# Kernel tuning notes

Measured on AMD Instinct MI355X. Metric: run time of the kernel, lower is better.

Reference implementation:

```python
import jax, jax.numpy as jnp
import numpy as np

N = 100000   # nodes
E = 1600000  # edges (avg degree 16)
D = 128      # input_dim == output_dim (residual requires equality)
BN_EPS = 1e-5


def setup_inputs() -> dict:
    key = jax.random.key(0)
    ks = jax.random.split(key, 8)
    X = jax.random.normal(ks[0], (N, D), dtype=jnp.float32)
    E_X = jax.random.normal(ks[1], (E, D), dtype=jnp.float32)
    snorm_n = jax.random.uniform(ks[2], (N, 1), dtype=jnp.float32)
    snorm_e = jax.random.uniform(ks[3], (E, 1), dtype=jnp.float32)
    src = jax.random.randint(ks[4], (E,), 0, N, dtype=jnp.int32)
    dst = jax.random.randint(ks[5], (E,), 0, N, dtype=jnp.int32)
    # Linear A and B parameters (torch nn.Linear: y = x @ W.T + b)
    scale = 1.0 / np.sqrt(D)
    A_w = jax.random.uniform(ks[6], (D, D), dtype=jnp.float32, minval=-scale, maxval=scale)
    B_w = jax.random.uniform(ks[7], (D, D), dtype=jnp.float32, minval=-scale, maxval=scale)
    A_b = jnp.zeros((D,), jnp.float32)
    B_b = jnp.zeros((D,), jnp.float32)
    # BatchNorm1d affine params (training mode -> batch stats)
    gamma = jnp.ones((D,), jnp.float32)
    beta = jnp.zeros((D,), jnp.float32)
    return {"X": X, "E_X": E_X, "snorm_n": snorm_n, "snorm_e": snorm_e,
            "src": src, "dst": dst, "A_w": A_w, "A_b": A_b,
            "B_w": B_w, "B_b": B_b, "gamma": gamma, "beta": beta}


def reference(X, E_X, snorm_n, snorm_e, src, dst, A_w, A_b, B_w, B_b, gamma, beta):
    AX = X @ A_w.T + A_b                       # [N, D]
    BX = X @ B_w.T + B_b                       # [N, D]
    # message: gather BX at edge sources; reduce: sum into destinations
    msgs = BX[src]                             # [E, D] irregular gather
    agg = jax.ops.segment_sum(msgs, dst, num_segments=N)  # [N, D]
    # DGL custom reduce only fires for nodes with in-degree > 0;
    # zero-in-degree nodes keep H = X
    indeg = jax.ops.segment_sum(jnp.ones((E,), X.dtype), dst, num_segments=N)
    H = jnp.where(indeg[:, None] > 0, AX + agg, X)
    H = H * snorm_n
    # BatchNorm1d (training mode: biased batch statistics)
    mean = jnp.mean(H, axis=0)
    var = jnp.mean((H - mean) ** 2, axis=0)
    H = (H - mean) * jax.lax.rsqrt(var + BN_EPS) * gamma + beta
    H = jax.nn.relu(H)
    H = X + H                                  # residual
    return (H, E_X)
```

## Files before the change

### kernel.cpp

```cpp
#include <hip/hip_runtime.h>

#define D 128
#define NNODES 100000
#define NEDGES 1600000
#define BN_EPS 1e-5f
#define NB_STATS 2048
#define NBLK_P 391
#define NTILES 1563

#define OFF_AX     0
#define OFF_BX16   12800000
#define OFF_ESRC   19200000
#define OFF_ORDER  20800000
#define OFF_INDEG  22400000
#define OFF_LEXC   22620000
#define OFF_BPART  22730000
#define OFF_BSCAN  22731000
#define OFF_PSUM   22740000
#define OFF_PSQ    23010000
#define OFF_SCALE  23280000
#define OFF_SHIFT  23280128
#define WS_NEED_BYTES 93200000ull

#define MAIN_GEMM 512
#define MAIN_EDGE 2048
#define MAIN_AGG  2048
#define MAIN_FIN  2048

typedef __attribute__((ext_vector_type(8))) short bf16x8;
typedef __attribute__((ext_vector_type(4))) float f32x4;

static __device__ __forceinline__ unsigned short f2bf(float f) {
    unsigned int u = __float_as_uint(f);
    u = (u + 0x7FFF + ((u >> 16) & 1)) >> 16;
    return (unsigned short)u;
}
static __device__ __forceinline__ float bf_lo(unsigned v) {
    return __uint_as_float(v << 16);
}
static __device__ __forceinline__ float bf_hi(unsigned v) {
    return __uint_as_float(v & 0xFFFF0000u);
}
static __device__ __forceinline__ bf16x8 pack8(float4 a, float4 b) {
    union { uint4 u; bf16x8 v; } r;
    r.u.x = (unsigned)f2bf(a.x) | ((unsigned)f2bf(a.y) << 16);
    r.u.y = (unsigned)f2bf(a.z) | ((unsigned)f2bf(a.w) << 16);
    r.u.z = (unsigned)f2bf(b.x) | ((unsigned)f2bf(b.y) << 16);
    r.u.w = (unsigned)f2bf(b.z) | ((unsigned)f2bf(b.w) << 16);
    return r.v;
}

__global__ __launch_bounds__(256, 2) void gemm2_kernel(
    const float* __restrict__ X,
    const float* __restrict__ Aw, const float* __restrict__ Ab,
    const float* __restrict__ Bw, const float* __restrict__ Bb,
    float* __restrict__ AX, unsigned short* __restrict__ BX16)
{
    __shared__ unsigned short Xs[64][136];

    const int w    = threadIdx.x >> 6;
    const int lane = threadIdx.x & 63;
    const bool isB = (w >> 1);
    const int colbase = (w & 1) * 64;
    const int bn   = lane & 15;
    const int kg   = lane >> 4;

    const float* __restrict__ Wm   = isB ? Bw : Aw;
    const float* __restrict__ bias = isB ? Bb : Ab;

    bf16x8 wf[4][4];
#pragma unroll
    for (int ks = 0; ks < 4; ++ks)
#pragma unroll
        for (int ct = 0; ct < 4; ++ct) {
            const int d = colbase + ct * 16 + bn;
            const int k = ks * 32 + kg * 8;
            const float4* wp = (const float4*)&Wm[d * D + k];
            wf[ks][ct] = pack8(wp[0], wp[1]);
        }

    float bias4[4];
#pragma unroll
    for (int ct = 0; ct < 4; ++ct) bias4[ct] = bias[colbase + ct * 16 + bn];

    for (int t = blockIdx.x; t < NTILES; t += MAIN_GEMM) {
        const int row0 = t * 64;
        for (int c = threadIdx.x; c < 1024; c += 256) {
            const int r   = c >> 4;
            const int col = (c & 15) * 8;
            const int row = min(row0 + r, NNODES - 1);
            const float4* xp = (const float4*)&X[(size_t)row * D + col];
            const float4 x0 = xp[0], x1 = xp[1];
            union { uint4 u; } pk;
            pk.u.x = (unsigned)f2bf(x0.x) | ((unsigned)f2bf(x0.y) << 16);
            pk.u.y = (unsigned)f2bf(x0.z) | ((unsigned)f2bf(x0.w) << 16);
            pk.u.z = (unsigned)f2bf(x1.x) | ((unsigned)f2bf(x1.y) << 16);
            pk.u.w = (unsigned)f2bf(x1.z) | ((unsigned)f2bf(x1.w) << 16);
            *(uint4*)&Xs[r][col] = pk.u;
        }
        __syncthreads();

        f32x4 acc[4][4];
#pragma unroll
        for (int rt = 0; rt < 4; ++rt)
#pragma unroll
            for (int ct = 0; ct < 4; ++ct)
                acc[rt][ct] = (f32x4){0.f, 0.f, 0.f, 0.f};

#pragma unroll
        for (int ks = 0; ks < 4; ++ks) {
            bf16x8 a[4];
#pragma unroll
            for (int rt = 0; rt < 4; ++rt)
                a[rt] = *(const bf16x8*)&Xs[rt * 16 + bn][ks * 32 + kg * 8];
#pragma unroll
            for (int rt = 0; rt < 4; ++rt)
#pragma unroll
                for (int ct = 0; ct < 4; ++ct)
                    acc[rt][ct] = __builtin_amdgcn_mfma_f32_16x16x32_bf16(
                        a[rt], wf[ks][ct], acc[rt][ct], 0, 0, 0);
        }
        __syncthreads();

#pragma unroll
        for (int rt = 0; rt < 4; ++rt) {
#pragma unroll
            for (int r = 0; r < 4; ++r) {
                const int row = row0 + rt * 16 + kg * 4 + r;
                if (row < NNODES) {
                    if (!isB) {
                        float* yrow = AX + (size_t)row * D + colbase;
#pragma unroll
                        for (int ct = 0; ct < 4; ++ct)
                            yrow[ct * 16 + bn] = acc[rt][ct][r] + bias4[ct];
                    } else {
                        unsigned short* yrow = BX16 + (size_t)row * D + colbase;
#pragma unroll
                        for (int ct = 0; ct < 4; ++ct)
                            yrow[ct * 16 + bn] =
                                f2bf(acc[rt][ct][r] + bias4[ct]);
                    }
                }
            }
        }
    }
}

__global__ __launch_bounds__(256) void hist_kernel(
    const int* __restrict__ dst, int* __restrict__ indeg,
    int* __restrict__ order)
{
    for (int e = blockIdx.x * 256 + threadIdx.x; e < NEDGES;
         e += MAIN_EDGE * 256)
        order[e] = atomicAdd(&indeg[dst[e]], 1);
}

__global__ __launch_bounds__(256) void scan1_kernel(
    const int* __restrict__ indeg, int* __restrict__ lexc,
    int* __restrict__ bpart)
{
    __shared__ int ls[256];
    const int i = blockIdx.x * 256 + threadIdx.x;
    const int v = (i < NNODES) ? indeg[i] : 0;
    ls[threadIdx.x] = v;
    __syncthreads();
    for (int off = 1; off < 256; off <<= 1) {
        int u = (threadIdx.x >= off) ? ls[threadIdx.x - off] : 0;
        __syncthreads();
        ls[threadIdx.x] += u;
        __syncthreads();
    }
    if (i < NNODES) lexc[i] = ls[threadIdx.x] - v;
    if (threadIdx.x == 255) bpart[blockIdx.x] = ls[255];
}

__global__ __launch_bounds__(512) void scan2_kernel(
    const int* __restrict__ bpart, int* __restrict__ bscan)
{
    __shared__ int ls[512];
    const int t = threadIdx.x;
    const int v = (t < NBLK_P) ? bpart[t] : 0;
    ls[t] = v;
    __syncthreads();
    for (int off = 1; off < 512; off <<= 1) {
        int u = (t >= off) ? ls[t - off] : 0;
        __syncthreads();
        ls[t] += u;
        __syncthreads();
    }
    if (t < NBLK_P) bscan[t] = ls[t] - v;
}

__global__ __launch_bounds__(256) void fill_kernel(
    const int* __restrict__ src, const int* __restrict__ dst,
    const int* __restrict__ bscan, const int* __restrict__ lexc,
    const int* __restrict__ order, int* __restrict__ esrc)
{
    for (int e = blockIdx.x * 256 + threadIdx.x; e < NEDGES;
         e += MAIN_EDGE * 256) {
        const int v = dst[e];
        esrc[bscan[v >> 8] + lexc[v] + order[e]] = src[e];
    }
}

__global__ __launch_bounds__(256, 8) void agg_kernel(
    const float4* __restrict__ AX4, const uint2* __restrict__ BX2,
    const float4* __restrict__ X4, const float* __restrict__ snorm,
    const int* __restrict__ bscan, const int* __restrict__ lexc,
    const int* __restrict__ indeg, const int* __restrict__ esrc,
    float4* __restrict__ Hpre4, float* __restrict__ psum,
    float* __restrict__ psq)
{
    const int w    = threadIdx.x >> 6;
    const int lane = threadIdx.x & 63;
    const int half = lane >> 5;
    const int hl   = lane & 31;
    float s0=0.f,s1=0.f,s2=0.f,s3=0.f, q0=0.f,q1=0.f,q2=0.f,q3=0.f;

    const int wid = blockIdx.x * 4 + w;
    for (int base = wid * 2; base < NNODES; base += MAIN_AGG * 8) {
        const int i = base + half;
        if (i < NNODES) {
            float a0, a1, a2, a3;
            const int deg = indeg[i];
            if (deg > 0) {
                const int rs = bscan[i >> 8] + lexc[i];
                float4 a = AX4[(size_t)i * 32 + hl];
                a0 = a.x; a1 = a.y; a2 = a.z; a3 = a.w;
                int e = rs;
                const int re = rs + deg;
                for (; e + 4 <= re; e += 4) {
                    const uint2 v0 = BX2[(size_t)esrc[e + 0] * 32 + hl];
                    const uint2 v1 = BX2[(size_t)esrc[e + 1] * 32 + hl];
                    const uint2 v2 = BX2[(size_t)esrc[e + 2] * 32 + hl];
                    const uint2 v3 = BX2[(size_t)esrc[e + 3] * 32 + hl];
                    a0 += bf_lo(v0.x)+bf_lo(v1.x)+bf_lo(v2.x)+bf_lo(v3.x);
                    a1 += bf_hi(v0.x)+bf_hi(v1.x)+bf_hi(v2.x)+bf_hi(v3.x);
                    a2 += bf_lo(v0.y)+bf_lo(v1.y)+bf_lo(v2.y)+bf_lo(v3.y);
                    a3 += bf_hi(v0.y)+bf_hi(v1.y)+bf_hi(v2.y)+bf_hi(v3.y);
                }
                for (; e < re; ++e) {
                    const uint2 v = BX2[(size_t)esrc[e] * 32 + hl];
                    a0 += bf_lo(v.x); a1 += bf_hi(v.x);
                    a2 += bf_lo(v.y); a3 += bf_hi(v.y);
                }
            } else {
                float4 x = X4[(size_t)i * 32 + hl];
                a0 = x.x; a1 = x.y; a2 = x.z; a3 = x.w;
            }
            const float sn = snorm[i];
            a0 *= sn; a1 *= sn; a2 *= sn; a3 *= sn;
            Hpre4[(size_t)i * 32 + hl] = make_float4(a0, a1, a2, a3);
            s0 += a0; s1 += a1; s2 += a2; s3 += a3;
            q0 += a0*a0; q1 += a1*a1; q2 += a2*a2; q3 += a3*a3;
        }
    }

    __shared__ float sp[4][64][4], sq[4][64][4];
    sp[w][lane][0]=s0; sp[w][lane][1]=s1; sp[w][lane][2]=s2; sp[w][lane][3]=s3;
    sq[w][lane][0]=q0; sq[w][lane][1]=q1; sq[w][lane][2]=q2; sq[w][lane][3]=q3;
    __syncthreads();
    if (threadIdx.x < D) {
        const int c  = threadIdx.x;
        const int l0 = c >> 2;
        const int j  = c & 3;
        float S = 0.f, Q = 0.f;
#pragma unroll
        for (int w2 = 0; w2 < 4; ++w2) {
            S += sp[w2][l0][j] + sp[w2][32 + l0][j];
            Q += sq[w2][l0][j] + sq[w2][32 + l0][j];
        }
        psum[blockIdx.x * D + c] = S;
        psq [blockIdx.x * D + c] = Q;
    }
}

__global__ __launch_bounds__(1024) void bnstats_kernel(
    const float* __restrict__ psum, const float* __restrict__ psq,
    const float* __restrict__ gamma, const float* __restrict__ beta,
    float* __restrict__ scale, float* __restrict__ shift)
{
    const int c = threadIdx.x & 127;
    const int g = threadIdx.x >> 7;
    float s = 0.f, q = 0.f;
    for (int b = g; b < NB_STATS; b += 8) {
        s += psum[b * D + c];
        q += psq [b * D + c];
    }
    __shared__ float ls[8][D], lq[8][D];
    ls[g][c] = s;
    lq[g][c] = q;
    __syncthreads();
    if (threadIdx.x < D) {
        float S = 0.f, Q = 0.f;
#pragma unroll
        for (int g2 = 0; g2 < 8; ++g2) { S += ls[g2][c]; Q += lq[g2][c]; }
        const float inv_n = 1.0f / (float)NNODES;
        float mean = S * inv_n;
        float var  = Q * inv_n - mean * mean;
        float sc   = rsqrtf(var + BN_EPS) * gamma[c];
        scale[c] = sc;
        shift[c] = beta[c] - mean * sc;
    }
}

__global__ __launch_bounds__(256) void final_kernel(
    const float* __restrict__ Hpre, const float* __restrict__ X,
    const float* __restrict__ scale, const float* __restrict__ shift,
    float* __restrict__ out)
{
    const int total = NNODES * D / 4;
    for (int i = blockIdx.x * 256 + threadIdx.x; i < total;
         i += MAIN_FIN * 256) {
        float4 h = ((const float4*)Hpre)[i];
        float4 x = ((const float4*)X)[i];
        int d0 = (i * 4) & 127;
        float4 r;
        r.x = x.x + fmaxf(0.f, h.x * scale[d0 + 0] + shift[d0 + 0]);
        r.y = x.y + fmaxf(0.f, h.y * scale[d0 + 1] + shift[d0 + 1]);
        r.z = x.z + fmaxf(0.f, h.z * scale[d0 + 2] + shift[d0 + 2]);
        r.w = x.w + fmaxf(0.f, h.w * scale[d0 + 3] + shift[d0 + 3]);
        ((float4*)out)[i] = r;
    }
}

extern "C" void kernel_launch(void* const* d_in, const int* in_sizes, int n_in,
                              void* d_out, int out_size, void* d_ws, size_t ws_size,
                              hipStream_t stream)
{
    const float* X       = (const float*)d_in[0];
    const float* E_X     = (const float*)d_in[1];
    const float* snorm_n = (const float*)d_in[2];
    const int*   src     = (const int*)d_in[4];
    const int*   dst     = (const int*)d_in[5];
    const float* A_w     = (const float*)d_in[6];
    const float* A_b     = (const float*)d_in[7];
    const float* B_w     = (const float*)d_in[8];
    const float* B_b     = (const float*)d_in[9];
    const float* gamma   = (const float*)d_in[10];
    const float* beta    = (const float*)d_in[11];

    float* out = (float*)d_out;
    const bool use_ws = (ws_size >= WS_NEED_BYTES);
    float* sb = use_ws ? (float*)d_ws : (out + (size_t)NNODES * D);

    float*          AX    = sb + OFF_AX;
    unsigned short* BX16  = (unsigned short*)(sb + OFF_BX16);
    int*            esrc  = (int*)(sb + OFF_ESRC);
    int*            order = (int*)(sb + OFF_ORDER);
    int*            indeg = (int*)(sb + OFF_INDEG);
    int*            lexc  = (int*)(sb + OFF_LEXC);
    int*            bpart = (int*)(sb + OFF_BPART);
    int*            bscan = (int*)(sb + OFF_BSCAN);
    float*          psum  = sb + OFF_PSUM;
    float*          psq   = sb + OFF_PSQ;
    float*          scale = sb + OFF_SCALE;
    float*          shift = sb + OFF_SHIFT;

    hipMemsetAsync(indeg, 0, NNODES * sizeof(int), stream);

    gemm2_kernel<<<MAIN_GEMM, 256, 0, stream>>>(
        X, A_w, A_b, B_w, B_b, AX, BX16);
    hist_kernel<<<MAIN_EDGE, 256, 0, stream>>>(dst, indeg, order);
    scan1_kernel<<<NBLK_P, 256, 0, stream>>>(indeg, lexc, bpart);
    scan2_kernel<<<1, 512, 0, stream>>>(bpart, bscan);
    fill_kernel<<<MAIN_EDGE, 256, 0, stream>>>(
        src, dst, bscan, lexc, order, esrc);
    agg_kernel<<<MAIN_AGG, 256, 0, stream>>>(
        (const float4*)AX, (const uint2*)BX16, (const float4*)X, snorm_n,
        bscan, lexc, indeg, esrc, (float4*)out, psum, psq);
    bnstats_kernel<<<1, 1024, 0, stream>>>(psum, psq, gamma, beta,
                                           scale, shift);
    final_kernel<<<MAIN_FIN, 256, 0, stream>>>(out, X, scale, shift, out);

    hipMemcpyAsync(out + (size_t)NNODES * D, E_X,
                   (size_t)NEDGES * D * sizeof(float),
                   hipMemcpyDeviceToDevice, stream);
}
```

Measured before the change: 659.4 us.

## Overlap E_X passthrough copy with compute kernels via dedicated copy blocks

Splits the 819 MB E_X passthrough copy into chunks, each handled by every eighth block of the hist, fill, agg and final kernels using nontemporal vector loads and stores. The remaining blocks do the original compute with adjusted strides, and only the tail goes through hipMemcpyAsync. The aim is to hide the bandwidth-bound copy behind latency-bound gather and atomic phases. In exchange the compute kernels have fewer blocks and compete with the copy for memory bandwidth, and the chunk offsets are hardcoded constants that must sum correctly.

Result: slower. 1.362 ms (+106.5%).

```diff
diff --git a/kernel.cpp b/kernel.cpp
--- a/kernel.cpp
+++ b/kernel.cpp
@@ -4,7 +4,7 @@
 #define NNODES 100000
 #define NEDGES 1600000
 #define BN_EPS 1e-5f
-#define NB_STATS 2048
+#define NB_STATS 1792
 #define NBLK_P 391
 #define NTILES 1563
 
@@ -23,12 +23,22 @@
 #define WS_NEED_BYTES 93200000ull
 
 #define MAIN_GEMM 512
-#define MAIN_EDGE 2048
-#define MAIN_AGG  2048
-#define MAIN_FIN  2048
+#define COMP_SM   1792
+#define GRID_HOST 2048
+
+#define CPY_HIST0   0L
+#define CPY_STR_SM  16384L
+#define CPY_FILL0   4194304L
+#define CPY_AGG0    8388608L
+#define CPY_STR_AGG 131072L
+#define CPY_FIN0    41943040L
+#define CPY_STR_FIN 8192L
+#define CPY_TAIL0   44040192L
+#define CPY_TOTAL   51200000L
 
 typedef __attribute__((ext_vector_type(8))) short bf16x8;
 typedef __attribute__((ext_vector_type(4))) float f32x4;
+typedef __attribute__((ext_vector_type(4))) unsigned int u32x4;
 
 static __device__ __forceinline__ unsigned short f2bf(float f) {
     unsigned int u = __float_as_uint(f);
@@ -48,6 +58,36 @@
     r.u.z = (unsigned)f2bf(b.x) | ((unsigned)f2bf(b.y) << 16);
     r.u.w = (unsigned)f2bf(b.z) | ((unsigned)f2bf(b.w) << 16);
     return r.v;
+}
+
+static __device__ __forceinline__ void copy_nt(
+    const u32x4* __restrict__ s, u32x4* __restrict__ d,
+    long base, long cnt)
+{
+    long i = base + threadIdx.x;
+    const long end = base + cnt;
+    for (; i + 7 * 256 < end; i += 8 * 256) {
+        u32x4 v0 = __builtin_nontemporal_load(&s[i + 0 * 256]);
+        u32x4 v1 = __builtin_nontemporal_load(&s[i + 1 * 256]);
+        u32x4 v2 = __builtin_nontemporal_load(&s[i + 2 * 256]);
+        u32x4 v3 = __builtin_nontemporal_load(&s[i + 3 * 256]);
+        u32x4 v4 = __builtin_nontemporal_load(&s[i + 4 * 256]);
+        u32x4 v5 = __builtin_nontemporal_load(&s[i + 5 * 256]);
+        u32x4 v6 = __builtin_nontemporal_load(&s[i + 6 * 256]);
+        u32x4 v7 = __builtin_nontemporal_load(&s[i + 7 * 256]);
+        __builtin_nontemporal_store(v0, &d[i + 0 * 256]);
+        __builtin_nontemporal_store(v1, &d[i + 1 * 256]);
+        __builtin_nontemporal_store(v2, &d[i + 2 * 256]);
+        __builtin_nontemporal_store(v3, &d[i + 3 * 256]);
+        __builtin_nontemporal_store(v4, &d[i + 4 * 256]);
+        __builtin_nontemporal_store(v5, &d[i + 5 * 256]);
+        __builtin_nontemporal_store(v6, &d[i + 6 * 256]);
+        __builtin_nontemporal_store(v7, &d[i + 7 * 256]);
+    }
+    for (; i < end; i += 256) {
+        u32x4 v = __builtin_nontemporal_load(&s[i]);
+        __builtin_nontemporal_store(v, &d[i]);
+    }
 }
 
 __global__ __launch_bounds__(256, 2) void gemm2_kernel(
@@ -148,10 +188,16 @@
 
 __global__ __launch_bounds__(256) void hist_kernel(
     const int* __restrict__ dst, int* __restrict__ indeg,
-    int* __restrict__ order)
-{
-    for (int e = blockIdx.x * 256 + threadIdx.x; e < NEDGES;
-         e += MAIN_EDGE * 256)
+    int* __restrict__ order,
+    const u32x4* __restrict__ exs, u32x4* __restrict__ exd, long cpb)
+{
+    if ((blockIdx.x & 7) == 7) {
+        if (cpb) copy_nt(exs, exd, CPY_HIST0 + (long)(blockIdx.x >> 3) * cpb,
+                         cpb);
+        return;
+    }
+    const int cb = blockIdx.x - (blockIdx.x >> 3);
+    for (int e = cb * 256 + threadIdx.x; e < NEDGES; e += COMP_SM * 256)
         order[e] = atomicAdd(&indeg[dst[e]], 1);
 }
 
@@ -194,10 +240,16 @@
 __global__ __launch_bounds__(256) void fill_kernel(
     const int* __restrict__ src, const int* __restrict__ dst,
     const int* __restrict__ bscan, const int* __restrict__ lexc,
-    const int* __restrict__ order, int* __restrict__ esrc)
-{
-    for (int e = blockIdx.x * 256 + threadIdx.x; e < NEDGES;
-         e += MAIN_EDGE * 256) {
+    const int* __restrict__ order, int* __restrict__ esrc,
+    const u32x4* __restrict__ exs, u32x4* __restrict__ exd, long cpb)
+{
+    if ((blockIdx.x & 7) == 7) {
+        if (cpb) copy_nt(exs, exd, CPY_FILL0 + (long)(blockIdx.x >> 3) * cpb,
+                         cpb);
+        return;
+    }
+    const int cb = blockIdx.x - (blockIdx.x >> 3);
+    for (int e = cb * 256 + threadIdx.x; e < NEDGES; e += COMP_SM * 256) {
         const int v = dst[e];
         esrc[bscan[v >> 8] + lexc[v] + order[e]] = src[e];
     }
@@ -209,16 +261,23 @@
     const int* __restrict__ bscan, const int* __restrict__ lexc,
     const int* __restrict__ indeg, const int* __restrict__ esrc,
     float4* __restrict__ Hpre4, float* __restrict__ psum,
-    float* __restrict__ psq)
-{
+    float* __restrict__ psq,
+    const u32x4* __restrict__ exs, u32x4* __restrict__ exd, long cpb)
+{
+    if ((blockIdx.x & 7) == 7) {
+        if (cpb) copy_nt(exs, exd, CPY_AGG0 + (long)(blockIdx.x >> 3) * cpb,
+                         cpb);
+        return;
+    }
+    const int cb   = blockIdx.x - (blockIdx.x >> 3);
     const int w    = threadIdx.x >> 6;
     const int lane = threadIdx.x & 63;
     const int half = lane >> 5;
     const int hl   = lane & 31;
     float s0=0.f,s1=0.f,s2=0.f,s3=0.f, q0=0.f,q1=0.f,q2=0.f,q3=0.f;
 
-    const int wid = blockIdx.x * 4 + w;
-    for (int base = wid * 2; base < NNODES; base += MAIN_AGG * 8) {
+    const int wid = cb * 4 + w;
+    for (int base = wid * 2; base < NNODES; base += COMP_SM * 8) {
         const int i = base + half;
         if (i < NNODES) {
             float a0, a1, a2, a3;
@@ -270,8 +329,8 @@
             S += sp[w2][l0][j] + sp[w2][32 + l0][j];
             Q += sq[w2][l0][j] + sq[w2][32 + l0][j];
         }
-        psum[blockIdx.x * D + c] = S;
-        psq [blockIdx.x * D + c] = Q;
+        psum[cb * D + c] = S;
+        psq [cb * D + c] = Q;
     }
 }
 
@@ -307,11 +366,17 @@
 __global__ __launch_bounds__(256) void final_kernel(
     const float* __restrict__ Hpre, const float* __restrict__ X,
     const float* __restrict__ scale, const float* __restrict__ shift,
-    float* __restrict__ out)
-{
+    float* __restrict__ out,
+    const u32x4* __restrict__ exs, u32x4* __restrict__ exd, long cpb)
+{
+    if ((blockIdx.x & 7) == 7) {
+        if (cpb) copy_nt(exs, exd, CPY_FIN0 + (long)(blockIdx.x >> 3) * cpb,
+                         cpb);
+        return;
+    }
+    const int cb = blockIdx.x - (blockIdx.x >> 3);
     const int total = NNODES * D / 4;
-    for (int i = blockIdx.x * 256 + threadIdx.x; i < total;
-         i += MAIN_FIN * 256) {
+    for (int i = cb * 256 + threadIdx.x; i < total; i += COMP_SM * 256) {
         float4 h = ((const float4*)Hpre)[i];
         float4 x = ((const float4*)X)[i];
         int d0 = (i * 4) & 127;
@@ -357,23 +422,34 @@
     float*          scale = sb + OFF_SCALE;
     float*          shift = sb + OFF_SHIFT;
 
+    const u32x4* exs = (const u32x4*)E_X;
+    u32x4*       exd = (u32x4*)(out + (size_t)NNODES * D);
+
+    const long cpb_sm   = use_ws ? CPY_STR_SM : 0;
+    const long cpb_agg  = use_ws ? CPY_STR_AGG : 0;
+    const long cpb_fin  = use_ws ? CPY_STR_FIN : 0;
+    const long tail_from = use_ws ? CPY_TAIL0 : 0;
+
     hipMemsetAsync(indeg, 0, NNODES * sizeof(int), stream);
 
     gemm2_kernel<<<MAIN_GEMM, 256, 0, stream>>>(
         X, A_w, A_b, B_w, B_b, AX, BX16);
-    hist_kernel<<<MAIN_EDGE, 256, 0, stream>>>(dst, indeg, order);
+    hist_kernel<<<GRID_HOST, 256, 0, stream>>>(
+        dst, indeg, order, exs, exd, cpb_sm);
     scan1_kernel<<<NBLK_P, 256, 0, stream>>>(indeg, lexc, bpart);
     scan2_kernel<<<1, 512, 0, stream>>>(bpart, bscan);
-    fill_kernel<<<MAIN_EDGE, 256, 0, stream>>>(
-        src, dst, bscan, lexc, order, esrc);
-    agg_kernel<<<MAIN_AGG, 256, 0, stream>>>(
+    fill_kernel<<<GRID_HOST, 256, 0, stream>>>(
+        src, dst, bscan, lexc, order, esrc, exs, exd, cpb_sm);
+    agg_kernel<<<GRID_HOST, 256, 0, stream>>>(
         (const float4*)AX, (const uint2*)BX16, (const float4*)X, snorm_n,
-        bscan, lexc, indeg, esrc, (float4*)out, psum, psq);
+        bscan, lexc, indeg, esrc, (float4*)out, psum, psq,
+        exs, exd, cpb_agg);
     bnstats_kernel<<<1, 1024, 0, stream>>>(psum, psq, gamma, beta,
                                            scale, shift);
-    final_kernel<<<MAIN_FIN, 256, 0, stream>>>(out, X, scale, shift, out);
-
-    hipMemcpyAsync(out + (size_t)NNODES * D, E_X,
-                   (size_t)NEDGES * D * sizeof(float),
+    final_kernel<<<GRID_HOST, 256, 0, stream>>>(
+        out, X, scale, shift, out, exs, exd, cpb_fin);
+
+    hipMemcpyAsync((float*)exd + tail_from * 4, E_X + tail_from * 4,
+                   (size_t)(CPY_TOTAL - tail_from) * 16,
                    hipMemcpyDeviceToDevice, stream);
 }
```
